# Kernel tuning notes

Hardware: AMD Instinct MI355X
Metric: run time of the kernel (lower is better)

Reference implementation:

```python
import jax, jax.numpy as jnp
import numpy as np

B, S, H, NH = 2, 2048, 1024, 16
HD = H // NH  # 64


def setup_inputs() -> dict:
    key = jax.random.key(0)
    ks = jax.random.split(key, 9)
    s = 1.0 / np.sqrt(H)
    d = {"x": jax.random.normal(ks[0], (B, S, H), jnp.float32)}
    for i, n in enumerate(["Wq", "Wk", "Wv", "Wo"]):
        d[n] = jax.random.normal(ks[1 + i], (H, H), jnp.float32) * s
    for i, n in enumerate(["bq", "bk", "bv", "bo"]):
        d[n] = jax.random.normal(ks[5 + i], (H,), jnp.float32) * s
    return d


def _heads(x, W, b):
    # torch nn.Linear: y = x @ W.T + b, then split heads -> (B, NH, S, HD)
    y = x @ W.T + b
    return y.reshape(B, S, NH, HD).transpose(0, 2, 1, 3)


def _tetra_channels(t):
    # tetrapoint vector [a, 1-a, a*(1-a), clamp(1-(a+(1-a)),0,1)] for a scalar slice t
    a = jax.nn.sigmoid(t)
    na = 1.0 - a
    neither = jnp.clip(1.0 - (a + na), 0.0, 1.0)
    return jnp.stack([a, na, a * na, neither], axis=-1)  # (..., 4)


def reference(x, Wq, bq, Wk, bk, Wv, bv, Wo, bo):
    Q = _heads(x, Wq, bq)  # (B, NH, S, HD)
    K = _heads(x, Wk, bk)
    V = _heads(x, Wv, bv)
    # Original indexes Q_tetrapoints[:, :, :, 0] on [B,NH,S,HD,4]: selects head-dim
    # slot 0 (resp. 2) and keeps the 4 tetrapoint channels -> (B, NH, S, 4).
    Qa = _tetra_channels(Q[..., 0])
    Ka = _tetra_channels(K[..., 0])
    Qb = _tetra_channels(Q[..., 2])
    Kb = _tetra_channels(K[..., 2])
    scores = (jnp.einsum('bhsc,bhtc->bhst', Qa, Ka) / np.sqrt(HD)
              + 0.1 * jnp.einsum('bhsc,bhtc->bhst', Qb, Kb))  # (B, NH, S, S)
    w = jax.nn.softmax(scores, axis=-1)
    out = jnp.einsum('bhst,bhtd->bhsd', w, V)  # (B, NH, S, HD)
    out = out.transpose(0, 2, 1, 3).reshape(B, S, H)
    return out @ Wo.T + bo
```

## Files before the change

kernel.cpp:

```cpp
#include <hip/hip_runtime.h>
#include <hip/hip_bf16.h>

#define SS 2048
#define HH 1024
#define NHH 16
#define HDD 64

using f32x4  = __attribute__((ext_vector_type(4))) float;
using bf16x8 = __attribute__((ext_vector_type(8))) short;

#if __has_builtin(__builtin_amdgcn_exp2f)
#define EXP2F __builtin_amdgcn_exp2f
#else
#define EXP2F exp2f
#endif

__device__ __forceinline__ unsigned short f2bf(float f) {
    unsigned u = __builtin_bit_cast(unsigned, f);
    unsigned r = u + 0x7FFFu + ((u >> 16) & 1u);
    return (unsigned short)(r >> 16);
}

__device__ __forceinline__ unsigned bfround(float f) {
    unsigned u = __builtin_bit_cast(unsigned, f);
    return u + 0x7FFFu + ((u >> 16) & 1u);
}
__device__ __forceinline__ unsigned pack2bf(float a, float b) {
    return __builtin_amdgcn_perm(bfround(b), bfround(a), 0x07060302u);
}
__device__ __forceinline__ unsigned pack2bf_trunc(float a, float b) {
    return __builtin_amdgcn_perm(__builtin_bit_cast(unsigned, b),
                                 __builtin_bit_cast(unsigned, a), 0x07060302u);
}

__device__ __forceinline__ void tetra(float t, float* c) {
    float a = 1.f / (1.f + __expf(-t));
    float na = 1.f - a;
    float nei = 1.f - (a + na);
    nei = fminf(fmaxf(nei, 0.f), 1.f);
    c[0] = a; c[1] = na; c[2] = a * na; c[3] = nei;
}

__device__ __forceinline__ void gll16(const unsigned short* g, unsigned short* l) {
    __builtin_amdgcn_global_load_lds(
        (const __attribute__((address_space(1))) unsigned int*)g,
        (__attribute__((address_space(3))) unsigned int*)l, 16, 0, 0);
}

__global__ __launch_bounds__(256) void cvt_kernel(
    const float* __restrict__ x, const float* __restrict__ Wv, const float* __restrict__ Wo,
    const float* __restrict__ Wq, const float* __restrict__ Wk,
    const float* __restrict__ bq, const float* __restrict__ bk,
    unsigned short* __restrict__ xb, unsigned short* __restrict__ Wvb, unsigned short* __restrict__ Wob,
    unsigned short* __restrict__ wselb, float* __restrict__ bselws)
{
    if (blockIdx.x >= 2048) {
        int n = blockIdx.x - 2048;
        int h = n >> 2, q = n & 3;
        int rowIdx = h * HDD + ((q & 1) ? 2 : 0);
        const float* src  = (q & 2) ? Wk : Wq;
        const float* bsrc = (q & 2) ? bk : bq;
        int t = threadIdx.x;
        float4 v = *(const float4*)(src + (size_t)rowIdx * HH + t * 4);
        uint2 pk;
        pk.x = pack2bf(v.x, v.y);
        pk.y = pack2bf(v.z, v.w);
        *(uint2*)(wselb + (size_t)n * HH + t * 4) = pk;
        if (t == 0) bselws[n] = bsrc[rowIdx];
        return;
    }
    size_t gid = (size_t)blockIdx.x * 256 + threadIdx.x;
    size_t base = gid * 8;
    {
        float4 a = *(const float4*)(x + base);
        float4 b = *(const float4*)(x + base + 4);
        uint4 pk;
        pk.x = pack2bf(a.x, a.y);
        pk.y = pack2bf(a.z, a.w);
        pk.z = pack2bf(b.x, b.y);
        pk.w = pack2bf(b.z, b.w);
        *(uint4*)(xb + base) = pk;
    }
    if (base < 1048576) {
        float4 a = *(const float4*)(Wv + base);
        float4 b = *(const float4*)(Wv + base + 4);
        uint4 pk;
        pk.x = pack2bf(a.x, a.y);
        pk.y = pack2bf(a.z, a.w);
        pk.z = pack2bf(b.x, b.y);
        pk.w = pack2bf(b.z, b.w);
        *(uint4*)(Wvb + base) = pk;
        a = *(const float4*)(Wo + base);
        b = *(const float4*)(Wo + base + 4);
        pk.x = pack2bf(a.x, a.y);
        pk.y = pack2bf(a.z, a.w);
        pk.z = pack2bf(b.x, b.y);
        pk.w = pack2bf(b.z, b.w);
        *(uint4*)(Wob + base) = pk;
    }
}

template<int OUT_MODE>
__device__ __forceinline__ void gemm_body(unsigned char* smem,
    const unsigned short* __restrict__ A, const unsigned short* __restrict__ Bw,
    const float* __restrict__ bias, void* __restrict__ Cout, int bx, int by)
{
    int tid = threadIdx.x;
    int wave = tid >> 6, lane = tid & 63;
    int l15 = lane & 15, l16 = lane >> 4;
    int wm = wave >> 1, wn = wave & 1;
    int m0 = by * 128, n0 = bx * 64;

    int lrow = lane >> 3;
    int lcolsw = ((lane & 7) ^ lrow) * 8;
    const unsigned short* Ag = A + (size_t)(m0 + wave * 32 + lrow) * HH + lcolsw;
    const unsigned short* Bg = Bw + (size_t)(n0 + wave * 16 + lrow) * HH + lcolsw;

    f32x4 acc[4][2] = {};

    {
        unsigned short* As = (unsigned short*)smem + (size_t)wave * 32 * 64;
        unsigned short* Bs = (unsigned short*)(smem + 16384) + (size_t)wave * 16 * 64;
        #pragma unroll
        for (int i = 0; i < 4; i++)
            gll16(Ag + (size_t)(i * 8) * HH, As + i * 8 * 64);
        #pragma unroll
        for (int i = 0; i < 2; i++)
            gll16(Bg + (size_t)(i * 8) * HH, Bs + i * 8 * 64);
    }
    __syncthreads();

    int swq = l15 & 7;
    int cur = 0;
    for (int k0 = 0; k0 < HH; k0 += 64) {
        if (k0 + 64 < HH) {
            unsigned char* nb = smem + (cur ^ 1) * 24576;
            unsigned short* As = (unsigned short*)nb + (size_t)wave * 32 * 64;
            unsigned short* Bs = (unsigned short*)(nb + 16384) + (size_t)wave * 16 * 64;
            #pragma unroll
            for (int i = 0; i < 4; i++)
                gll16(Ag + (size_t)(i * 8) * HH + k0 + 64, As + i * 8 * 64);
            #pragma unroll
            for (int i = 0; i < 2; i++)
                gll16(Bg + (size_t)(i * 8) * HH + k0 + 64, Bs + i * 8 * 64);
        }

        unsigned char* cb = smem + cur * 24576;
        #pragma unroll
        for (int kk = 0; kk < 2; kk++) {
            int csw = ((kk * 4 + l16) ^ swq) * 16;
            bf16x8 af[4], bfr[2];
            #pragma unroll
            for (int mi = 0; mi < 4; mi++)
                af[mi] = *(const bf16x8*)(cb + (wm * 64 + mi * 16 + l15) * 128 + csw);
            #pragma unroll
            for (int ni = 0; ni < 2; ni++)
                bfr[ni] = *(const bf16x8*)(cb + 16384 + (wn * 32 + ni * 16 + l15) * 128 + csw);
            #pragma unroll
            for (int mi = 0; mi < 4; mi++)
                #pragma unroll
                for (int ni = 0; ni < 2; ni++)
                    acc[mi][ni] = __builtin_amdgcn_mfma_f32_16x16x32_bf16(af[mi], bfr[ni], acc[mi][ni], 0, 0, 0);
        }
        __syncthreads();
        cur ^= 1;
    }

    float bv[2];
    #pragma unroll
    for (int ni = 0; ni < 2; ni++)
        bv[ni] = bias[n0 + wn * 32 + ni * 16 + l15];

    #pragma unroll
    for (int mi = 0; mi < 4; mi++) {
        #pragma unroll
        for (int ni = 0; ni < 2; ni++) {
            int n = n0 + wn * 32 + ni * 16 + l15;
            if (OUT_MODE == 0) {
                #pragma unroll
                for (int r = 0; r < 4; r++) {
                    int m = m0 + wm * 64 + mi * 16 + l16 * 4 + r;
                    ((float*)Cout)[(size_t)m * HH + n] = acc[mi][ni][r] + bv[ni];
                }
            } else {
                int m = m0 + wm * 64 + mi * 16 + l16 * 4;
                int b = m >> 11, s = m & 2047;
                int h = n >> 6, d = n & 63;
                uint2 pk;
                pk.x = pack2bf(acc[mi][ni][0] + bv[ni], acc[mi][ni][1] + bv[ni]);
                pk.y = pack2bf(acc[mi][ni][2] + bv[ni], acc[mi][ni][3] + bv[ni]);
                *(uint2*)((unsigned short*)Cout + ((size_t)((b * NHH + h) * HDD + d)) * SS + s) = pk;
            }
        }
    }
}

__device__ __forceinline__ void qk_body(unsigned char* smem,
    const unsigned short* __restrict__ xb, const unsigned short* __restrict__ wselb,
    const float* __restrict__ bselws,
    unsigned short* __restrict__ qfb, unsigned short* __restrict__ kfb, int blk)
{
    auto xs = (unsigned short (*)[72])smem;
    auto ws = (unsigned short (*)[72])(smem + 4608);
    auto ys = (float (*)[68])(smem + 13824);
    int tid = threadIdx.x;
    int wave = tid >> 6, lane = tid & 63;
    int l15 = lane & 15, l16 = lane >> 4;
    int m0 = blk * 32;
    int n0w = wave * 16;

    int xr = tid >> 3, xseg = (tid & 7) * 8;
    int wr = tid >> 2, wseg = (tid & 3) * 16;
    const unsigned short* xp = xb + (size_t)(m0 + xr) * HH + xseg;
    const unsigned short* wp = wselb + (size_t)wr * HH + wseg;

    f32x4 acc[2] = {};

    uint4 xv  = *(const uint4*)(xp);
    uint4 wv0 = *(const uint4*)(wp);
    uint4 wv1 = *(const uint4*)(wp + 8);

    for (int k0 = 0; k0 < HH; k0 += 64) {
        __syncthreads();
        *(uint4*)&xs[xr][xseg] = xv;
        *(uint4*)&ws[wr][wseg]     = wv0;
        *(uint4*)&ws[wr][wseg + 8] = wv1;
        __syncthreads();

        int kn = (k0 + 64) & (HH - 1);
        uint4 nxv  = *(const uint4*)(xp + kn);
        uint4 nwv0 = *(const uint4*)(wp + kn);
        uint4 nwv1 = *(const uint4*)(wp + kn + 8);

        #pragma unroll
        for (int kk = 0; kk < 64; kk += 32) {
            bf16x8 bfr = *(const bf16x8*)&ws[n0w + l15][kk + l16 * 8];
            #pragma unroll
            for (int mi = 0; mi < 2; mi++) {
                bf16x8 af = *(const bf16x8*)&xs[mi * 16 + l15][kk + l16 * 8];
                acc[mi] = __builtin_amdgcn_mfma_f32_16x16x32_bf16(af, bfr, acc[mi], 0, 0, 0);
            }
        }
        xv = nxv; wv0 = nwv0; wv1 = nwv1;
    }

    float bias = bselws[n0w + l15];
    __syncthreads();
    #pragma unroll
    for (int mi = 0; mi < 2; mi++)
        #pragma unroll
        for (int r = 0; r < 4; r++)
            ys[mi * 16 + l16 * 4 + r][n0w + l15] = acc[mi][r] + bias;
    __syncthreads();

    #pragma unroll
    for (int pass = 0; pass < 2; pass++) {
        int ml = tid & 31;
        int h = (tid >> 5) + pass * 8;
        float4 y4 = *(const float4*)&ys[ml][h * 4];
        float qa[4], qb2[4], ka[4], kb2[4];
        tetra(y4.x, qa);
        tetra(y4.y, qb2);
        tetra(y4.z, ka);
        tetra(y4.w, kb2);
        int m = m0 + ml, b = m >> 11, s = m & 2047;
        size_t base = ((size_t)(b * NHH + h) * SS + s) * 8;
        const float sA = 0.18033688011112042f;
        const float sB = 0.14426950408889634f;
        uint4 qp, kp;
        qp.x = pack2bf(qa[0] * sA, qa[1] * sA);
        qp.y = pack2bf(qa[2] * sA, qa[3] * sA);
        qp.z = pack2bf(qb2[0] * sB, qb2[1] * sB);
        qp.w = pack2bf(qb2[2] * sB, qb2[3] * sB);
        kp.x = pack2bf(ka[0], ka[1]);
        kp.y = pack2bf(ka[2], ka[3]);
        kp.z = pack2bf(kb2[0], kb2[1]);
        kp.w = pack2bf(kb2[2], kb2[3]);
        *(uint4*)(qfb + base) = qp;
        *(uint4*)(kfb + base) = kp;
    }
}

__global__ __launch_bounds__(256) void fused_mid(
    const unsigned short* __restrict__ xb,
    const unsigned short* __restrict__ Wvb, const float* __restrict__ bv,
    unsigned short* __restrict__ Vt,
    const unsigned short* __restrict__ wselb, const float* __restrict__ bselws,
    unsigned short* __restrict__ qfb, unsigned short* __restrict__ kfb)
{
    __shared__ __align__(16) unsigned char smem[49152];
    int p = blockIdx.x;
    if (p < 512) {
        int id = (p & 7) * 64 + (p >> 3);
        gemm_body<2>(smem, xb, Wvb, bv, Vt, id & 15, id >> 4);
    } else {
        int q = p - 512;
        int id = (q & 7) * 16 + (q >> 3);
        qk_body(smem, xb, wselb, bselws, qfb, kfb, id);
    }
}

__global__ __launch_bounds__(256) void gemm_out(
    const unsigned short* __restrict__ A, const unsigned short* __restrict__ Bw,
    const float* __restrict__ bias, float* __restrict__ Cout)
{
    __shared__ __align__(16) unsigned char smem[49152];
    int p = blockIdx.x;
    int id = (p & 7) * 64 + (p >> 3);
    gemm_body<0>(smem, A, Bw, bias, Cout, id & 15, id >> 4);
}

__global__ __launch_bounds__(256) void attn_mfma(
    const unsigned short* __restrict__ qfb, const unsigned short* __restrict__ kfb,
    const unsigned short* __restrict__ Vt, unsigned short* __restrict__ attnb)
{
    __shared__ __align__(16) unsigned char lds[32768];

    int tid = threadIdx.x;
    int wave = tid >> 6, lane = tid & 63;
    int l15 = lane & 15, l16 = lane >> 4;
    int l7 = l15 & 7;

    int L = blockIdx.x + (blockIdx.y << 4);
    int logical = ((L & 7) << 6) + (L >> 3);
    int bh = logical >> 4, qblk = logical & 15;
    int b = bh >> 4, h = bh & 15;
    int s0 = qblk * 128 + wave * 32;

    bf16x8 qA = {0,0,0,0,0,0,0,0}, qB = {0,0,0,0,0,0,0,0};
    if (l16 == 0) {
        qA = *(const bf16x8*)(qfb + ((size_t)bh * SS + s0 + l15) * 8);
        qB = *(const bf16x8*)(qfb + ((size_t)bh * SS + s0 + 16 + l15) * 8);
    }

    const short oneb = 0x3F80;
    bf16x8 ones = {oneb,oneb,oneb,oneb,oneb,oneb,oneb,oneb};

    const unsigned short* kfA = kfb + ((size_t)bh * SS + l15) * 8;
    int vd = tid >> 2, vr = tid & 3;
    const unsigned short* vsrc = Vt + ((size_t)bh * HDD + vd) * SS + vr * 16;

    unsigned char* vrow = lds + vd * 128;
    int sw0 = ((vr * 2)     ^ (vd & 7)) << 4;
    int sw1 = ((vr * 2 + 1) ^ (vd & 7)) << 4;
    unsigned char* psw = lds + 16384 + wave * 4096;

    f32x4 acc[2][4] = {};
    f32x4 accl[2] = {};

    {
        uint4 t0a = *(const uint4*)(vsrc);
        uint4 t0b = *(const uint4*)(vsrc + 8);
        *(uint4*)(vrow + sw0) = t0a;
        *(uint4*)(vrow + sw1) = t0b;
    }
    uint4 sv0 = *(const uint4*)(vsrc + 64);
    uint4 sv1 = *(const uint4*)(vsrc + 64 + 8);
    bf16x8 kfr[4];
    #pragma unroll
    for (int tb = 0; tb < 4; tb++)
        kfr[tb] = *(const bf16x8*)(kfA + (size_t)(tb * 16) * 8);

    for (int it = 0; it < 32; it++) {
        int t0 = it << 6;
        __syncthreads();

        int nb = (it + 1) & 1;
        *(uint4*)(vrow + nb * 8192 + sw0) = sv0;
        *(uint4*)(vrow + nb * 8192 + sw1) = sv1;

        int tv = (t0 + 128) & (SS - 1);
        uint4 nv0 = *(const uint4*)(vsrc + tv);
        uint4 nv1 = *(const uint4*)(vsrc + tv + 8);
        int tkf = (t0 + 64) & (SS - 1);
        bf16x8 nkf[4];
        #pragma unroll
        for (int tb = 0; tb < 4; tb++)
            nkf[tb] = *(const bf16x8*)(kfA + (size_t)(tkf + tb * 16) * 8);

        #pragma unroll
        for (int g = 0; g < 2; g++) {
            bf16x8 qf = g ? qB : qA;
            #pragma unroll
            for (int tb = 0; tb < 4; tb++) {
                f32x4 sc = {};
                sc = __builtin_amdgcn_mfma_f32_16x16x32_bf16(kfr[tb], qf, sc, 0, 0, 0);
                uint2 pw;
                pw.x = pack2bf_trunc(EXP2F(sc[0]), EXP2F(sc[1]));
                pw.y = pack2bf_trunc(EXP2F(sc[2]), EXP2F(sc[3]));
                int qr = g * 16 + l15;
                int c  = (tb * 2 + (l16 >> 1)) ^ l7;
                *(uint2*)(psw + qr * 128 + c * 16 + (l16 & 1) * 8) = pw;
            }
        }

        int cb = it & 1;
        unsigned char* vbuf = lds + cb * 8192;
        __builtin_amdgcn_s_setprio(1);
        #pragma unroll
        for (int tk = 0; tk < 2; tk++) {
            int csw = ((tk * 4 + l16) ^ l7) << 4;
            bf16x8 apA = *(const bf16x8*)(psw + l15 * 128 + csw);
            bf16x8 apB = *(const bf16x8*)(psw + (16 + l15) * 128 + csw);
            accl[0] = __builtin_amdgcn_mfma_f32_16x16x32_bf16(apA, ones, accl[0], 0, 0, 0);
            accl[1] = __builtin_amdgcn_mfma_f32_16x16x32_bf16(apB, ones, accl[1], 0, 0, 0);
            #pragma unroll
            for (int nd = 0; nd < 4; nd++) {
                bf16x8 bv = *(const bf16x8*)(vbuf + (nd * 16 + l15) * 128 + csw);
                acc[0][nd] = __builtin_amdgcn_mfma_f32_16x16x32_bf16(apA, bv, acc[0][nd], 0, 0, 0);
                acc[1][nd] = __builtin_amdgcn_mfma_f32_16x16x32_bf16(apB, bv, acc[1][nd], 0, 0, 0);
            }
        }
        __builtin_amdgcn_s_setprio(0);

        sv0 = nv0; sv1 = nv1;
        #pragma unroll
        for (int tb = 0; tb < 4; tb++) kfr[tb] = nkf[tb];
    }

    #pragma unroll
    for (int g = 0; g < 2; g++) {
        #pragma unroll
        for (int r = 0; r < 4; r++) {
            float linv = 1.f / accl[g][r];
            int q = s0 + g * 16 + l16 * 4 + r;
            size_t row = (size_t)(b * SS + q) * HH + h * HDD;
            #pragma unroll
            for (int nd = 0; nd < 4; nd++)
                attnb[row + nd * 16 + l15] = f2bf(acc[g][nd][r] * linv);
        }
    }
}

extern "C" void kernel_launch(void* const* d_in, const int* in_sizes, int n_in,
                              void* d_out, int out_size, void* d_ws, size_t ws_size,
                              hipStream_t stream)
{
    const float* x  = (const float*)d_in[0];
    const float* Wq = (const float*)d_in[1];
    const float* Wk = (const float*)d_in[2];
    const float* Wv = (const float*)d_in[3];
    const float* Wo = (const float*)d_in[4];
    const float* bq = (const float*)d_in[5];
    const float* bk = (const float*)d_in[6];
    const float* bv = (const float*)d_in[7];
    const float* bo = (const float*)d_in[8];

    unsigned short* qfb   = (unsigned short*)d_ws;
    unsigned short* kfb   = qfb + 524288;
    unsigned short* xb    = kfb + 524288;
    unsigned short* attnb = xb;
    unsigned short* Wvb   = xb + 4194304;
    unsigned short* Wob   = Wvb + 1048576;
    unsigned short* Vt    = Wob + 1048576;
    unsigned short* wselb  = Vt + 4194304;
    float*          bselws = (float*)(wselb + 65536);

    cvt_kernel<<<2112, 256, 0, stream>>>(x, Wv, Wo, Wq, Wk, bq, bk, xb, Wvb, Wob, wselb, bselws);
    fused_mid<<<640, 256, 0, stream>>>(xb, Wvb, bv, Vt, wselb, bselws, qfb, kfb);
    attn_mfma<<<dim3(16, 32), 256, 0, stream>>>(qfb, kfb, Vt, attnb);
    gemm_out<<<512, 256, 0, stream>>>(attnb, Wob, bo, (float*)d_out);
}
```

Baseline: 158.0 us.

## Software-pipeline attention loop: overlap QK/exp of tile i with PV of tile i-1

The P tile in LDS becomes double-buffered per wave. The PV MFMAs for the previous key tile now run after the QK scores and exp of the current tile, with a single barrier placed after them. The aim is to let exp/VALU work and global prefetches overlap the matrix-core work instead of serialising them behind the barrier. This raises LDS per block from 32KB to 48KB, which may lower the number of resident blocks, and adds an epilogue that handles the last tile.

```diff
diff --git a/kernel.cpp b/kernel.cpp
--- a/kernel.cpp
+++ b/kernel.cpp
@@ -314,7 +314,7 @@
     const unsigned short* __restrict__ qfb, const unsigned short* __restrict__ kfb,
     const unsigned short* __restrict__ Vt, unsigned short* __restrict__ attnb)
 {
-    __shared__ __align__(16) unsigned char lds[32768];
+    __shared__ __align__(16) unsigned char lds[49152];
 
     int tid = threadIdx.x;
     int wave = tid >> 6, lane = tid & 63;
@@ -343,7 +343,7 @@
     unsigned char* vrow = lds + vd * 128;
     int sw0 = ((vr * 2)     ^ (vd & 7)) << 4;
     int sw1 = ((vr * 2 + 1) ^ (vd & 7)) << 4;
-    unsigned char* psw = lds + 16384 + wave * 4096;
+    unsigned char* psbase = lds + 16384 + wave * 8192;
 
     f32x4 acc[2][4] = {};
     f32x4 accl[2] = {};
@@ -363,21 +363,17 @@
 
     for (int it = 0; it < 32; it++) {
         int t0 = it << 6;
-        __syncthreads();
-
-        int nb = (it + 1) & 1;
-        *(uint4*)(vrow + nb * 8192 + sw0) = sv0;
-        *(uint4*)(vrow + nb * 8192 + sw1) = sv1;
-
+
+        int tkf = (t0 + 64) & (SS - 1);
+        bf16x8 nkf[4];
+        #pragma unroll
+        for (int tb = 0; tb < 4; tb++)
+            nkf[tb] = *(const bf16x8*)(kfA + (size_t)(tkf + tb * 16) * 8);
         int tv = (t0 + 128) & (SS - 1);
         uint4 nv0 = *(const uint4*)(vsrc + tv);
         uint4 nv1 = *(const uint4*)(vsrc + tv + 8);
-        int tkf = (t0 + 64) & (SS - 1);
-        bf16x8 nkf[4];
-        #pragma unroll
-        for (int tb = 0; tb < 4; tb++)
-            nkf[tb] = *(const bf16x8*)(kfA + (size_t)(tkf + tb * 16) * 8);
-
+
+        unsigned char* psw = psbase + (it & 1) * 4096;
         #pragma unroll
         for (int g = 0; g < 2; g++) {
             bf16x8 qf = g ? qB : qA;
@@ -394,14 +390,48 @@
             }
         }
 
-        int cb = it & 1;
-        unsigned char* vbuf = lds + cb * 8192;
-        __builtin_amdgcn_s_setprio(1);
+        if (it > 0) {
+            unsigned char* vbuf = lds + ((it - 1) & 1) * 8192;
+            unsigned char* psr = psbase + ((it - 1) & 1) * 4096;
+            __builtin_amdgcn_s_setprio(1);
+            #pragma unroll
+            for (int tk = 0; tk < 2; tk++) {
+                int csw = ((tk * 4 + l16) ^ l7) << 4;
+                bf16x8 apA = *(const bf16x8*)(psr + l15 * 128 + csw);
+                bf16x8 apB = *(const bf16x8*)(psr + (16 + l15) * 128 + csw);
+                accl[0] = __builtin_amdgcn_mfma_f32_16x16x32_bf16(apA, ones, accl[0], 0, 0, 0);
+                accl[1] = __builtin_amdgcn_mfma_f32_16x16x32_bf16(apB, ones, accl[1], 0, 0, 0);
+                #pragma unroll
+                for (int nd = 0; nd < 4; nd++) {
+                    bf16x8 bv = *(const bf16x8*)(vbuf + (nd * 16 + l15) * 128 + csw);
+                    acc[0][nd] = __builtin_amdgcn_mfma_f32_16x16x32_bf16(apA, bv, acc[0][nd], 0, 0, 0);
+                    acc[1][nd] = __builtin_amdgcn_mfma_f32_16x16x32_bf16(apB, bv, acc[1][nd], 0, 0, 0);
+                }
+            }
+            __builtin_amdgcn_s_setprio(0);
+        }
+
+        __syncthreads();
+
+        if (it < 31) {
+            int nb = (it + 1) & 1;
+            *(uint4*)(vrow + nb * 8192 + sw0) = sv0;
+            *(uint4*)(vrow + nb * 8192 + sw1) = sv1;
+        }
+
+        sv0 = nv0; sv1 = nv1;
+        #pragma unroll
+        for (int tb = 0; tb < 4; tb++) kfr[tb] = nkf[tb];
+    }
+
+    {
+        unsigned char* vbuf = lds + 8192;
+        unsigned char* psr = psbase + 4096;
         #pragma unroll
         for (int tk = 0; tk < 2; tk++) {
             int csw = ((tk * 4 + l16) ^ l7) << 4;
-            bf16x8 apA = *(const bf16x8*)(psw + l15 * 128 + csw);
-            bf16x8 apB = *(const bf16x8*)(psw + (16 + l15) * 128 + csw);
+            bf16x8 apA = *(const bf16x8*)(psr + l15 * 128 + csw);
+            bf16x8 apB = *(const bf16x8*)(psr + (16 + l15) * 128 + csw);
             accl[0] = __builtin_amdgcn_mfma_f32_16x16x32_bf16(apA, ones, accl[0], 0, 0, 0);
             accl[1] = __builtin_amdgcn_mfma_f32_16x16x32_bf16(apB, ones, accl[1], 0, 0, 0);
             #pragma unroll
@@ -411,11 +441,6 @@
                 acc[1][nd] = __builtin_amdgcn_mfma_f32_16x16x32_bf16(apB, bv, acc[1][nd], 0, 0, 0);
             }
         }
-        __builtin_amdgcn_s_setprio(0);
-
-        sv0 = nv0; sv1 = nv1;
-        #pragma unroll
-        for (int tb = 0; tb < 4; tb++) kfr[tb] = nkf[tb];
     }
 
     #pragma unroll
```

Result: no change. 156.9 us (-0.7%).

## Split attention key range across two wave groups with LDS reduction

Applied to the files above, without the earlier changes.

Doubles the attention block to 512 threads, with two groups of four waves each processing half of the key sequence (1024 keys, 16 iterations) for the same 128 queries. Each half has its own double-buffered V tile in LDS. At the end, the partial numerators and denominators are summed through LDS before normalization and the store. This halves the serial loop length per wave and adds parallelism. The cost is double the LDS (64KB), which may lower occupancy, plus an extra reduction step with syncs.

```diff
diff --git a/kernel.cpp b/kernel.cpp
--- a/kernel.cpp
+++ b/kernel.cpp
@@ -310,14 +310,15 @@
     gemm_body<0>(smem, A, Bw, bias, Cout, id & 15, id >> 4);
 }
 
-__global__ __launch_bounds__(256) void attn_mfma(
+__global__ __launch_bounds__(512) void attn_mfma(
     const unsigned short* __restrict__ qfb, const unsigned short* __restrict__ kfb,
     const unsigned short* __restrict__ Vt, unsigned short* __restrict__ attnb)
 {
-    __shared__ __align__(16) unsigned char lds[32768];
+    __shared__ __align__(16) unsigned char lds[65536];
 
     int tid = threadIdx.x;
     int wave = tid >> 6, lane = tid & 63;
+    int sub = wave & 3, hf = wave >> 2;
     int l15 = lane & 15, l16 = lane >> 4;
     int l7 = l15 & 7;
 
@@ -325,7 +326,7 @@
     int logical = ((L & 7) << 6) + (L >> 3);
     int bh = logical >> 4, qblk = logical & 15;
     int b = bh >> 4, h = bh & 15;
-    int s0 = qblk * 128 + wave * 32;
+    int s0 = qblk * 128 + sub * 32;
 
     bf16x8 qA = {0,0,0,0,0,0,0,0}, qB = {0,0,0,0,0,0,0,0};
     if (l16 == 0) {
@@ -336,14 +337,16 @@
     const short oneb = 0x3F80;
     bf16x8 ones = {oneb,oneb,oneb,oneb,oneb,oneb,oneb,oneb};
 
-    const unsigned short* kfA = kfb + ((size_t)bh * SS + l15) * 8;
-    int vd = tid >> 2, vr = tid & 3;
-    const unsigned short* vsrc = Vt + ((size_t)bh * HDD + vd) * SS + vr * 16;
-
-    unsigned char* vrow = lds + vd * 128;
+    const unsigned short* kfA = kfb + ((size_t)bh * SS + hf * 1024 + l15) * 8;
+
+    int t8 = tid & 255, shf = tid >> 8;
+    int vd = t8 >> 2, vr = t8 & 3;
+    const unsigned short* vsrc = Vt + ((size_t)bh * HDD + vd) * SS + shf * 1024 + vr * 16;
+
+    unsigned char* vrow = lds + shf * 16384 + vd * 128;
     int sw0 = ((vr * 2)     ^ (vd & 7)) << 4;
     int sw1 = ((vr * 2 + 1) ^ (vd & 7)) << 4;
-    unsigned char* psw = lds + 16384 + wave * 4096;
+    unsigned char* psw = lds + 32768 + wave * 4096;
 
     f32x4 acc[2][4] = {};
     f32x4 accl[2] = {};
@@ -361,18 +364,17 @@
     for (int tb = 0; tb < 4; tb++)
         kfr[tb] = *(const bf16x8*)(kfA + (size_t)(tb * 16) * 8);
 
-    for (int it = 0; it < 32; it++) {
-        int t0 = it << 6;
+    for (int it = 0; it < 16; it++) {
         __syncthreads();
 
         int nb = (it + 1) & 1;
         *(uint4*)(vrow + nb * 8192 + sw0) = sv0;
         *(uint4*)(vrow + nb * 8192 + sw1) = sv1;
 
-        int tv = (t0 + 128) & (SS - 1);
+        int tv = ((it + 2) & 15) << 6;
         uint4 nv0 = *(const uint4*)(vsrc + tv);
         uint4 nv1 = *(const uint4*)(vsrc + tv + 8);
-        int tkf = (t0 + 64) & (SS - 1);
+        int tkf = ((it + 1) & 15) << 6;
         bf16x8 nkf[4];
         #pragma unroll
         for (int tb = 0; tb < 4; tb++)
@@ -394,8 +396,7 @@
             }
         }
 
-        int cb = it & 1;
-        unsigned char* vbuf = lds + cb * 8192;
+        unsigned char* vbuf = lds + hf * 16384 + (it & 1) * 8192;
         __builtin_amdgcn_s_setprio(1);
         #pragma unroll
         for (int tk = 0; tk < 2; tk++) {
@@ -418,16 +419,40 @@
         for (int tb = 0; tb < 4; tb++) kfr[tb] = nkf[tb];
     }
 
-    #pragma unroll
-    for (int g = 0; g < 2; g++) {
-        #pragma unroll
-        for (int r = 0; r < 4; r++) {
-            float linv = 1.f / accl[g][r];
-            int q = s0 + g * 16 + l16 * 4 + r;
-            size_t row = (size_t)(b * SS + q) * HH + h * HDD;
+    __syncthreads();
+    float* xch = (float*)lds;
+    if (wave >= 4) {
+        float* dst = xch + ((size_t)((wave - 4) * 64 + lane)) * 40;
+        #pragma unroll
+        for (int g = 0; g < 2; g++)
             #pragma unroll
             for (int nd = 0; nd < 4; nd++)
-                attnb[row + nd * 16 + l15] = f2bf(acc[g][nd][r] * linv);
+                *(f32x4*)(dst + (g * 4 + nd) * 4) = acc[g][nd];
+        *(f32x4*)(dst + 32) = accl[0];
+        *(f32x4*)(dst + 36) = accl[1];
+    }
+    __syncthreads();
+    if (wave < 4) {
+        float* src = xch + ((size_t)(wave * 64 + lane)) * 40;
+        #pragma unroll
+        for (int g = 0; g < 2; g++)
+            #pragma unroll
+            for (int nd = 0; nd < 4; nd++)
+                acc[g][nd] += *(const f32x4*)(src + (g * 4 + nd) * 4);
+        accl[0] += *(const f32x4*)(src + 32);
+        accl[1] += *(const f32x4*)(src + 36);
+
+        #pragma unroll
+        for (int g = 0; g < 2; g++) {
+            #pragma unroll
+            for (int r = 0; r < 4; r++) {
+                float linv = 1.f / accl[g][r];
+                int q = s0 + g * 16 + l16 * 4 + r;
+                size_t row = (size_t)(b * SS + q) * HH + h * HDD;
+                #pragma unroll
+                for (int nd = 0; nd < 4; nd++)
+                    attnb[row + nd * 16 + l15] = f2bf(acc[g][nd][r] * linv);
+            }
         }
     }
 }
@@ -458,6 +483,6 @@
 
     cvt_kernel<<<2112, 256, 0, stream>>>(x, Wv, Wo, Wq, Wk, bq, bk, xb, Wvb, Wob, wselb, bselws);
     fused_mid<<<640, 256, 0, stream>>>(xb, Wvb, bv, Vt, wselb, bselws, qfb, kfb);
-    attn_mfma<<<dim3(16, 32), 256, 0, stream>>>(qfb, kfb, Vt, attnb);
+    attn_mfma<<<dim3(16, 32), 512, 0, stream>>>(qfb, kfb, Vt, attnb);
     gemm_out<<<512, 256, 0, stream>>>(attnb, Wob, bo, (float*)d_out);
 }
```

Result: faster. 149.5 us, median of 2 (-5.4%).
